# Performance work log

Measured on AMD Instinct MI355X. Metric: run time of the kernel, lower is better.

## Reference

```python
import jax, jax.numpy as jnp
import numpy as np

B, T, I, H = 64, 512, 512, 1024


def setup_inputs() -> dict:
    key = jax.random.key(0)
    k1, k2, k3, k4, k5, k6 = jax.random.split(key, 6)
    s = 1.0 / np.sqrt(H)  # PyTorch LSTMCell init scale
    return {
        "sequence": jax.random.normal(k1, (B, T, I), dtype=jnp.float32),
        "original_lengths": jax.random.randint(k2, (B,), 0, T, dtype=jnp.int32),
        "W_ih": jax.random.uniform(k3, (4 * H, I), minval=-s, maxval=s, dtype=jnp.float32),
        "W_hh": jax.random.uniform(k4, (4 * H, H), minval=-s, maxval=s, dtype=jnp.float32),
        "b_ih": jax.random.uniform(k5, (4 * H,), minval=-s, maxval=s, dtype=jnp.float32),
        "b_hh": jax.random.uniform(k6, (4 * H,), minval=-s, maxval=s, dtype=jnp.float32),
    }


def reference(sequence, original_lengths, W_ih, W_hh, b_ih, b_hh):
    b, t_max, _ = sequence.shape
    h0 = jnp.zeros((b, H), dtype=sequence.dtype)
    c0 = jnp.zeros((b, H), dtype=sequence.dtype)
    last0 = jnp.zeros((b, H), dtype=sequence.dtype)
    bias = b_ih + b_hh

    # Precompute input-side gate projections for all timesteps in one big GEMM.
    # gates_x: [T, B, 4H]
    gates_x = jnp.einsum('bti,gi->tbg', sequence, W_ih) + bias

    def step(carry, inp):
        h, c, last = carry
        gx, t = inp
        gates = gx + h @ W_hh.T  # [B, 4H], PyTorch gate order i,f,g,o
        i, f, g, o = jnp.split(gates, 4, axis=-1)
        i = jax.nn.sigmoid(i)
        f = jax.nn.sigmoid(f)
        g = jnp.tanh(g)
        o = jax.nn.sigmoid(o)
        c = f * c + i * g
        h = o * jnp.tanh(c)
        last = jnp.where((original_lengths > t)[:, None], h, last)
        return (h, c, last), None

    ts = jnp.arange(t_max, dtype=jnp.int32)
    (h, c, last_hidden), _ = jax.lax.scan(step, (h0, c0, last0), (gates_x, ts))
    return last_hidden
```

## Files before the change

### kernel.cpp

```cpp
#include <hip/hip_runtime.h>


typedef short bf16x8 __attribute__((ext_vector_type(8)));
typedef float f32x4  __attribute__((ext_vector_type(4)));
typedef unsigned u32x4 __attribute__((ext_vector_type(4)));

#define BB 64
#define TT 512
#define II 512
#define HH 1024

#define NBLK 256
#define NTHR 512

#define WS_CNT_OFF   0
#define WS_HPAKH_OFF 8192
#define WS_HPAKL_OFF (8192 + 262144)
#define WS_XPAKH_OFF (1 << 20)
#define WS_XPAKL_OFF ((1 << 20) + (32u << 20))

#define HBUF_STRIDE 65536
#define XT_STRIDE   32768

__device__ __forceinline__ int atomic_add_rlx(int* p) {
    return __hip_atomic_fetch_add(p, 1, __ATOMIC_RELAXED, __HIP_MEMORY_SCOPE_AGENT);
}
__device__ __forceinline__ int load_rlx(const int* p) {
    return __hip_atomic_load(p, __ATOMIC_RELAXED, __HIP_MEMORY_SCOPE_AGENT);
}
__device__ __forceinline__ void store_wt_u16(unsigned short* p, unsigned short v) {
    __hip_atomic_store(p, v, __ATOMIC_RELAXED, __HIP_MEMORY_SCOPE_AGENT);
}

__device__ __forceinline__ float fast_sigmoid(float x) {
    return 1.0f / (1.0f + __expf(-x));
}
__device__ __forceinline__ float fast_tanh(float x) {
    x = fminf(15.0f, fmaxf(-15.0f, x));
    const float e = __expf(2.0f * x);
    return (e - 1.0f) / (e + 1.0f);
}

__device__ __forceinline__ void split_bf16(float x, unsigned& hi, unsigned& lo)
{
    unsigned b = __float_as_uint(x);
    hi = (b + 0x7fffu + ((b >> 16) & 1u)) >> 16;
    float r = x - __uint_as_float(hi << 16);
    unsigned bl = __float_as_uint(r);
    lo = (bl + 0x7fffu + ((bl >> 16) & 1u)) >> 16;
}

#define MFMA(A, B, C) __builtin_amdgcn_mfma_f32_16x16x32_bf16((A), (B), (C), 0, 0, 0)

__device__ __forceinline__ void issue_coh(const unsigned short* p, u32x4& d)
{
    asm volatile("global_load_dwordx4 %0, %1, off sc0 sc1" : "=v"(d) : "v"(p));
}
#define WAITSTG8(FH, FL)                                                      \
    asm volatile("s_waitcnt vmcnt(0)"                                         \
        : "+v"(FH[0]), "+v"(FH[1]), "+v"(FH[2]), "+v"(FH[3]),                 \
          "+v"(FL[0]), "+v"(FL[1]), "+v"(FL[2]), "+v"(FL[3])                  \
        :: "memory")

__global__ void __launch_bounds__(256)
transpose_pack_x(const float* __restrict__ x,
                 unsigned short* __restrict__ xH, unsigned short* __restrict__ xL)
{
    __shared__ float tile[64][65];
    const int t   = (int)blockIdx.x;
    const int tid = (int)threadIdx.x;
    const int li  = tid & 63;
    const int w4  = tid >> 6;

    for (int kc = 0; kc < II; kc += 64) {
#pragma unroll
        for (int r = 0; r < 16; ++r) {
            const int b = w4 * 16 + r;
            tile[b][li] = x[((size_t)b * TT + t) * II + kc + li];
        }
        __syncthreads();
#pragma unroll
        for (int half = 0; half < 2; ++half) {
            const int u  = tid + half * 256;
            const int k8 = u >> 6, b = u & 63;
            unsigned short oh[8], ol[8];
#pragma unroll
            for (int e = 0; e < 8; ++e) {
                unsigned hi, lo;
                split_bf16(tile[b][k8 * 8 + e], hi, lo);
                oh[e] = (unsigned short)hi;
                ol[e] = (unsigned short)lo;
            }
            const size_t idx = (size_t)t * XT_STRIDE + ((kc >> 3) + k8) * 512 + b * 8;
            *(uint4*)(xH + idx) = *(const uint4*)oh;
            *(uint4*)(xL + idx) = *(const uint4*)ol;
        }
        __syncthreads();
    }
}

__global__ void __launch_bounds__(NTHR, 2)
lstm_mfma(const unsigned short* __restrict__ xH,
          const unsigned short* __restrict__ xL,
          const int*   __restrict__ lens,
          const float* __restrict__ Wih,
          const float* __restrict__ Whh,
          const float* __restrict__ bih,
          const float* __restrict__ bhh,
          unsigned short* __restrict__ hH,
          unsigned short* __restrict__ hL,
          int*   __restrict__ cnts,
          float* __restrict__ out)
{
    __shared__ float red[2][2][3][2][16][17];
    __shared__ unsigned short hstg[2][128][128];
    __shared__ float biaslds[4][16];
    __shared__ int hflag;

    const int tid  = (int)threadIdx.x;
    const int l    = tid & 63;
    const int p    = __builtin_amdgcn_readfirstlane(tid >> 6);
    const int kh   = p & 3;
    const int mt   = p >> 2;
    const int bsub = l & 15;
    const int q    = l >> 4;

    const int jt = (int)blockIdx.x >> 2;
    const int bq = (int)blockIdx.x & 3;
    const int j0 = jt * 16;
    const int b0 = bq * 16;

    const int bofs = (b0 + bsub) * 8;

    int*       prodc = cnts + (bq * 4 + (jt >> 4)) * 64;
    const int* pollc = cnts + (bq * 4 + (l & 3)) * 64;

    bf16x8 whi[2][12], wlo[2][12];
#pragma unroll
    for (int u = 0; u < 2; ++u) {
        const int row = (l & 3) * HH + j0 + (mt * 2 + u) * 4 + ((l & 15) >> 2);
#pragma unroll
        for (int kt = 0; kt < 12; ++kt) {
            const int ktg = (kt < 4) ? (4 * kh + kt) : (16 + 8 * kh + (kt - 4));
            const float* src = (ktg < 16)
                ? (Wih + (size_t)row * II + ktg * 32 + q * 8)
                : (Whh + (size_t)row * HH + (ktg - 16) * 32 + q * 8);
            const float4 w0 = *(const float4*)src;
            const float4 w1 = *(const float4*)(src + 4);
            const float wf[8] = {w0.x, w0.y, w0.z, w0.w, w1.x, w1.y, w1.z, w1.w};
#pragma unroll
            for (int e = 0; e < 8; ++e) {
                unsigned hi, lo;
                split_bf16(wf[e], hi, lo);
                whi[u][kt][e] = (short)hi;
                wlo[u][kt][e] = (short)lo;
            }
        }
    }

    float c[2] = {0.f, 0.f}, lasth[2] = {0.f, 0.f};
    int len = 0;
    const size_t hchunk = (size_t)(2 * jt + mt) * 512;

    if (kh == 0) {
        len = lens[b0 + bsub];
#pragma unroll
        for (int u = 0; u < 2; ++u) {
            store_wt_u16(hH + hchunk + bofs + 4 * u + q, 0);
            store_wt_u16(hL + hchunk + bofs + 4 * u + q, 0);
        }
        asm volatile("s_waitcnt vmcnt(0)" ::: "memory");
        if (l == 0) atomic_add_rlx(prodc);
    }

    if (tid < 64) {
        const int gi = tid >> 4, jj = tid & 15;
        biaslds[gi][jj] = bih[gi * HH + j0 + jj] + bhh[gi * HH + j0 + jj];
    }
    if (tid == 0)
        __hip_atomic_store(&hflag, 0, __ATOMIC_RELAXED, __HIP_MEMORY_SCOPE_WORKGROUP);
    __syncthreads();

    for (int t = 0; t < TT; ++t) {
        f32x4 s0[2], s12[2];
#pragma unroll
        for (int u = 0; u < 2; ++u)
            s0[u] = s12[u] = (f32x4){0.f, 0.f, 0.f, 0.f};
        {
            const unsigned short* xh = xH + (size_t)t * XT_STRIDE;
            const unsigned short* xl = xL + (size_t)t * XT_STRIDE;
#pragma unroll
            for (int xi = 0; xi < 4; ++xi) {
                const int idx = ((4 * kh + xi) * 4 + q) * 512 + bofs;
                const bf16x8 ahi = *(const bf16x8*)(xh + idx);
                const bf16x8 alo = *(const bf16x8*)(xl + idx);
#pragma unroll
                for (int u = 0; u < 2; ++u) {
                    s0[u]  = MFMA(whi[u][xi], ahi, s0[u]);
                    s12[u] = MFMA(whi[u][xi], alo, s12[u]);
                    s12[u] = MFMA(wlo[u][xi], ahi, s12[u]);
                }
            }
        }

        {
            const int need = 32 * (t + 1);
            if (p == 7) {
                while (load_rlx(pollc) < need)
                    __builtin_amdgcn_s_sleep(1);
                if (l == 0)
                    __hip_atomic_store(&hflag, t + 1, __ATOMIC_RELAXED,
                                       __HIP_MEMORY_SCOPE_WORKGROUP);
            } else {
                while (__hip_atomic_load(&hflag, __ATOMIC_RELAXED,
                                         __HIP_MEMORY_SCOPE_WORKGROUP) < t + 1)
                    __builtin_amdgcn_s_sleep(1);
            }
            asm volatile("" ::: "memory");
        }

        const unsigned short* hph = hH + (t & 1) * HBUF_STRIDE;
        const unsigned short* hpl = hL + (t & 1) * HBUF_STRIDE;
        {
            u32x4 fh[4], fl[4];
#pragma unroll
            for (int r = 0; r < 4; ++r) {
                const int chunk = kh * 32 + mt * 16 + r * 4 + q;
                const int idx = chunk * 512 + bofs;
                issue_coh(hph + idx, fh[r]);
                issue_coh(hpl + idx, fl[r]);
            }
            WAITSTG8(fh, fl);
#pragma unroll
            for (int r = 0; r < 4; ++r) {
                const int chunk = kh * 32 + mt * 16 + r * 4 + q;
                *(u32x4*)&hstg[0][chunk][bsub * 8] = fh[r];
                *(u32x4*)&hstg[1][chunk][bsub * 8] = fl[r];
            }
        }
        __syncthreads();

#pragma unroll
        for (int hi2 = 0; hi2 < 8; ++hi2) {
            const int chunk = kh * 32 + hi2 * 4 + q;
            const bf16x8 ahi = *(const bf16x8*)&hstg[0][chunk][bsub * 8];
            const bf16x8 alo = *(const bf16x8*)&hstg[1][chunk][bsub * 8];
#pragma unroll
            for (int u = 0; u < 2; ++u) {
                s0[u]  = MFMA(whi[u][4 + hi2], ahi, s0[u]);
                s12[u] = MFMA(whi[u][4 + hi2], alo, s12[u]);
                s12[u] = MFMA(wlo[u][4 + hi2], ahi, s12[u]);
            }
        }

        f32x4 acc[2];
#pragma unroll
        for (int u = 0; u < 2; ++u) acc[u] = s0[u] + s12[u];
        const int pa = t & 1;

        if (kh != 0) {
#pragma unroll
            for (int u = 0; u < 2; ++u)
#pragma unroll
                for (int i = 0; i < 4; ++i)
                    red[pa][mt][kh - 1][u][bsub][4 * q + i] = acc[u][i];
        }
        __syncthreads();

        if (kh == 0) {
            unsigned short* dsth = hH + ((t + 1) & 1) * HBUF_STRIDE + hchunk;
            unsigned short* dstl = hL + ((t + 1) & 1) * HBUF_STRIDE + hchunk;
#pragma unroll
            for (int u = 0; u < 2; ++u) {
                const int jj = (mt * 2 + u) * 4 + q;
                float g4[4];
#pragma unroll
                for (int i = 0; i < 4; ++i)
                    g4[i] = acc[u][i] + biaslds[i][jj]
                          + red[pa][mt][0][u][bsub][4 * q + i]
                          + red[pa][mt][1][u][bsub][4 * q + i]
                          + red[pa][mt][2][u][bsub][4 * q + i];
                const float ig = fast_sigmoid(g4[0]);
                const float fg = fast_sigmoid(g4[1]);
                const float gg = fast_tanh(g4[2]);
                const float og = fast_sigmoid(g4[3]);
                c[u] = fg * c[u] + ig * gg;
                const float h = og * fast_tanh(c[u]);
                unsigned hi, lo;
                split_bf16(h, hi, lo);
                store_wt_u16(dsth + bofs + 4 * u + q, (unsigned short)hi);
                store_wt_u16(dstl + bofs + 4 * u + q, (unsigned short)lo);
                if (t == len - 1) lasth[u] = h;
            }
            asm volatile("s_waitcnt vmcnt(0)" ::: "memory");
            if (l == 0) atomic_add_rlx(prodc);
        }
    }

    if (kh == 0) {
#pragma unroll
        for (int u = 0; u < 2; ++u) {
            const int jj = (mt * 2 + u) * 4 + q;
            out[(size_t)(b0 + bsub) * HH + j0 + jj] = lasth[u];
        }
    }
}

extern "C" void kernel_launch(void* const* d_in, const int* in_sizes, int n_in,
                              void* d_out, int out_size, void* d_ws, size_t ws_size,
                              hipStream_t stream)
{
    const float* seq  = (const float*)d_in[0];
    const int*   lens = (const int*)  d_in[1];
    const float* Wih  = (const float*)d_in[2];
    const float* Whh  = (const float*)d_in[3];
    const float* bih  = (const float*)d_in[4];
    const float* bhh  = (const float*)d_in[5];
    float* out = (float*)d_out;

    char* ws = (char*)d_ws;
    int*            cnts = (int*)           (ws + WS_CNT_OFF);
    unsigned short* hH   = (unsigned short*)(ws + WS_HPAKH_OFF);
    unsigned short* hL   = (unsigned short*)(ws + WS_HPAKL_OFF);
    unsigned short* xH   = (unsigned short*)(ws + WS_XPAKH_OFF);
    unsigned short* xL   = (unsigned short*)(ws + WS_XPAKL_OFF);

    hipMemsetAsync(cnts, 0, 8192, stream);
    transpose_pack_x<<<dim3(TT), dim3(256), 0, stream>>>(seq, xH, xL);
    lstm_mfma<<<dim3(NBLK), dim3(NTHR), 0, stream>>>(xH, xL, lens, Wih, Whh, bih, bhh,
                                                     hH, hL, cnts, out);
}
```

Baseline: 2.461 ms.

## Replace contended atomic counters with per-block flags polled by a full wavefront

The cross-block step barrier no longer has every producer block atomically increment one of a few shared counters. Each block now writes its step number to its own padded flag word, and the consumer wave polls 64 flags at once, one per lane. Publication also moves to after the next step's input MFMAs, with an LDS handshake between the two kh==0 waves, so that the store drain overlaps compute. The goal is to remove atomic contention and serialization on the hot counters, at the cost of a wider poll and a delayed, more intricate publish ordering.

```diff
diff --git a/kernel.cpp b/kernel.cpp
--- a/kernel.cpp
+++ b/kernel.cpp
@@ -13,20 +13,20 @@
 #define NBLK 256
 #define NTHR 512
 
-#define WS_CNT_OFF   0
-#define WS_HPAKH_OFF 8192
-#define WS_HPAKL_OFF (8192 + 262144)
+#define WS_FLAG_OFF  0
+#define WS_HPAKH_OFF 16384
+#define WS_HPAKL_OFF (16384 + 262144)
 #define WS_XPAKH_OFF (1 << 20)
 #define WS_XPAKL_OFF ((1 << 20) + (32u << 20))
 
 #define HBUF_STRIDE 65536
 #define XT_STRIDE   32768
 
-__device__ __forceinline__ int atomic_add_rlx(int* p) {
-    return __hip_atomic_fetch_add(p, 1, __ATOMIC_RELAXED, __HIP_MEMORY_SCOPE_AGENT);
-}
 __device__ __forceinline__ int load_rlx(const int* p) {
     return __hip_atomic_load(p, __ATOMIC_RELAXED, __HIP_MEMORY_SCOPE_AGENT);
+}
+__device__ __forceinline__ void store_rlx_int(int* p, int v) {
+    __hip_atomic_store(p, v, __ATOMIC_RELAXED, __HIP_MEMORY_SCOPE_AGENT);
 }
 __device__ __forceinline__ void store_wt_u16(unsigned short* p, unsigned short v) {
     __hip_atomic_store(p, v, __ATOMIC_RELAXED, __HIP_MEMORY_SCOPE_AGENT);
@@ -109,13 +109,14 @@
           const float* __restrict__ bhh,
           unsigned short* __restrict__ hH,
           unsigned short* __restrict__ hL,
-          int*   __restrict__ cnts,
+          int*   __restrict__ flags,
           float* __restrict__ out)
 {
     __shared__ float red[2][2][3][2][16][17];
     __shared__ unsigned short hstg[2][128][128];
     __shared__ float biaslds[4][16];
     __shared__ int hflag;
+    __shared__ int pubsync[2][2];
 
     const int tid  = (int)threadIdx.x;
     const int l    = tid & 63;
@@ -132,8 +133,8 @@
 
     const int bofs = (b0 + bsub) * 8;
 
-    int*       prodc = cnts + (bq * 4 + (jt >> 4)) * 64;
-    const int* pollc = cnts + (bq * 4 + (l & 3)) * 64;
+    int*       myflag = flags + (bq * 64 + jt) * 16;
+    const int* pollf  = flags + bq * 1024;
 
     bf16x8 whi[2][12], wlo[2][12];
 #pragma unroll
@@ -169,16 +170,19 @@
             store_wt_u16(hH + hchunk + bofs + 4 * u + q, 0);
             store_wt_u16(hL + hchunk + bofs + 4 * u + q, 0);
         }
-        asm volatile("s_waitcnt vmcnt(0)" ::: "memory");
-        if (l == 0) atomic_add_rlx(prodc);
     }
 
     if (tid < 64) {
         const int gi = tid >> 4, jj = tid & 15;
         biaslds[gi][jj] = bih[gi * HH + j0 + jj] + bhh[gi * HH + j0 + jj];
     }
-    if (tid == 0)
+    if (tid == 0) {
         __hip_atomic_store(&hflag, 0, __ATOMIC_RELAXED, __HIP_MEMORY_SCOPE_WORKGROUP);
+        __hip_atomic_store(&pubsync[0][0], 0, __ATOMIC_RELAXED, __HIP_MEMORY_SCOPE_WORKGROUP);
+        __hip_atomic_store(&pubsync[0][1], 0, __ATOMIC_RELAXED, __HIP_MEMORY_SCOPE_WORKGROUP);
+        __hip_atomic_store(&pubsync[1][0], 0, __ATOMIC_RELAXED, __HIP_MEMORY_SCOPE_WORKGROUP);
+        __hip_atomic_store(&pubsync[1][1], 0, __ATOMIC_RELAXED, __HIP_MEMORY_SCOPE_WORKGROUP);
+    }
     __syncthreads();
 
     for (int t = 0; t < TT; ++t) {
@@ -203,10 +207,22 @@
             }
         }
 
+        if (kh == 0) {
+            asm volatile("s_waitcnt vmcnt(0)" ::: "memory");
+            if (l == 0)
+                __hip_atomic_store(&pubsync[t & 1][mt], t + 1, __ATOMIC_RELAXED,
+                                   __HIP_MEMORY_SCOPE_WORKGROUP);
+            if (mt == 0 && l == 0) {
+                while (__hip_atomic_load(&pubsync[t & 1][1], __ATOMIC_RELAXED,
+                                         __HIP_MEMORY_SCOPE_WORKGROUP) < t + 1)
+                    __builtin_amdgcn_s_sleep(1);
+                store_rlx_int(myflag, t + 1);
+            }
+        }
+
         {
-            const int need = 32 * (t + 1);
             if (p == 7) {
-                while (load_rlx(pollc) < need)
+                while (load_rlx(pollf + l * 16) < t + 1)
                     __builtin_amdgcn_s_sleep(1);
                 if (l == 0)
                     __hip_atomic_store(&hflag, t + 1, __ATOMIC_RELAXED,
@@ -292,8 +308,6 @@
                 store_wt_u16(dstl + bofs + 4 * u + q, (unsigned short)lo);
                 if (t == len - 1) lasth[u] = h;
             }
-            asm volatile("s_waitcnt vmcnt(0)" ::: "memory");
-            if (l == 0) atomic_add_rlx(prodc);
         }
     }
 
@@ -319,14 +333,14 @@
     float* out = (float*)d_out;
 
     char* ws = (char*)d_ws;
-    int*            cnts = (int*)           (ws + WS_CNT_OFF);
-    unsigned short* hH   = (unsigned short*)(ws + WS_HPAKH_OFF);
-    unsigned short* hL   = (unsigned short*)(ws + WS_HPAKL_OFF);
-    unsigned short* xH   = (unsigned short*)(ws + WS_XPAKH_OFF);
-    unsigned short* xL   = (unsigned short*)(ws + WS_XPAKL_OFF);
-
-    hipMemsetAsync(cnts, 0, 8192, stream);
+    int*            flags = (int*)           (ws + WS_FLAG_OFF);
+    unsigned short* hH    = (unsigned short*)(ws + WS_HPAKH_OFF);
+    unsigned short* hL    = (unsigned short*)(ws + WS_HPAKL_OFF);
+    unsigned short* xH    = (unsigned short*)(ws + WS_XPAKH_OFF);
+    unsigned short* xL    = (unsigned short*)(ws + WS_XPAKL_OFF);
+
+    hipMemsetAsync(flags, 0, 16384, stream);
     transpose_pack_x<<<dim3(TT), dim3(256), 0, stream>>>(seq, xH, xL);
     lstm_mfma<<<dim3(NBLK), dim3(NTHR), 0, stream>>>(xH, xL, lens, Wih, Whh, bih, bhh,
-                                                     hH, hL, cnts, out);
-}
+                                                     hH, hL, flags, out);
+}
```

Measured after the change: 3.166 ms. 1.29x slower.
